# Kernel optimization log

Hardware: AMD Instinct MI355X
Metric: run time of the kernel (lower is better)

The kernel has to match this reference:

```python
import jax, jax.numpy as jnp
import numpy as np
import math

B, T, C = 1, 2048, 2048
NH, HS = 16, 128          # hs = C // nh
NLQ, NLKV, DHR = 1536, 512, 64


def _rope(x, cos, sin):
    # x: [B, T, H, D]; cos/sin: [T, D//2]. Rotates pairs (even, odd) like
    # torch's complex-multiply apply_rotary_emb.
    xr = x.reshape(x.shape[:-1] + (-1, 2))
    x_re, x_im = xr[..., 0], xr[..., 1]
    c = cos[None, :, None, :]
    s = sin[None, :, None, :]
    out = jnp.stack([x_re * c - x_im * s, x_re * s + x_im * c], axis=-1)
    return out.reshape(x.shape)


def setup_inputs() -> dict:
    key = jax.random.key(0)
    ks = jax.random.split(key, 9)
    sc = 0.02  # init scale so logits stay sane
    x = jax.random.normal(ks[0], (B, T, C), jnp.float32)
    # RoPE tables (theta = 10000), matching precompute_freqs_cis
    inv = 1.0 / (10000.0 ** (jnp.arange(0, DHR, 2, dtype=jnp.float32) / DHR))
    ang = jnp.outer(jnp.arange(T, dtype=jnp.float32), inv)  # [T, DHR//2]
    return {
        "x": x,
        "freqs_cos": jnp.cos(ang),
        "freqs_sin": jnp.sin(ang),
        "W_dq": jax.random.normal(ks[1], (NLQ, C), jnp.float32) * sc,
        "W_uq": jax.random.normal(ks[2], (C, NLQ), jnp.float32) * sc,
        "W_dkv": jax.random.normal(ks[3], (NLKV, C), jnp.float32) * sc,
        "W_uk": jax.random.normal(ks[4], (C, NLKV), jnp.float32) * sc,
        "W_uv": jax.random.normal(ks[5], (C, NLKV), jnp.float32) * sc,
        "W_qr": jax.random.normal(ks[6], (NH * DHR, NLQ), jnp.float32) * sc,
        "W_kr": jax.random.normal(ks[7], (DHR, C), jnp.float32) * sc,
        "W_o": jax.random.normal(ks[8], (C, C), jnp.float32) * sc,
    }


def reference(x, freqs_cos, freqs_sin, W_dq, W_uq, W_dkv, W_uk, W_uv, W_qr, W_kr, W_o):
    # ---- low-rank query/kv down-projections ----
    c_q = x @ W_dq.T                       # [B,T,NLQ]
    c_kv = x @ W_dkv.T                     # [B,T,NLKV]  (no kv_cache: c_kv = new_c_kv)

    # ---- weight absorption (training path) ----
    # torch: W_uq.weight.view(1,nlq,nh,hs).transpose(1,2) @ W_uk.weight.view(1,nh,hs,nlkv)
    Wuq_h = W_uq.reshape(NLQ, NH, HS).transpose(1, 0, 2)   # [NH,NLQ,HS]
    Wuk_h = W_uk.reshape(NH, HS, NLKV)                     # [NH,HS,NLKV]
    k_eff = jnp.einsum('hql,hlk->hqk', Wuq_h, Wuk_h)       # [NH,NLQ,NLKV]
    # torch: (W_uv.weight.T @ W_o.weight.T).view(nlkv,nh,hs).transpose(0,1)
    v_eff = (W_uv.T @ W_o.T).reshape(NLKV, NH, HS).transpose(1, 0, 2)  # [NH,NLKV,HS]

    # ---- content attention scores in latent space ----
    attn_c = jnp.einsum('bhtk,bsk->bhts',
                        jnp.einsum('btq,hqk->bhtk', c_q, k_eff), c_kv)  # [B,NH,T,T]

    # ---- decoupled RoPE subspace ----
    k_r = _rope((x @ W_kr.T)[:, :, None, :], freqs_cos, freqs_sin)[:, :, 0, :]   # [B,T,DHR]
    q_r = _rope((c_q @ W_qr.T).reshape(B, T, NH, DHR), freqs_cos, freqs_sin)
    q_r = q_r.transpose(0, 2, 1, 3)                                              # [B,NH,T,DHR]
    attn_r = jnp.einsum('bhtd,bsd->bhts', q_r, k_r)                              # [B,NH,T,T]

    # ---- combine, causal mask, softmax ----
    scale = 1.0 / math.sqrt(HS + DHR)
    scores = (attn_c + attn_r) * scale
    causal = jnp.tril(jnp.ones((T, T), dtype=bool))  # mask = triu(diag=1) complement
    scores = jnp.where(causal[None, None], scores, jnp.float32(-jnp.inf))
    attn = jax.nn.softmax(scores, axis=-1)           # dropout p=0.0

    # ---- value path: attend in latent space, then absorbed up+output proj ----
    y_lat = jnp.einsum('bhts,bsk->bhtk', attn, c_kv)          # [B,NH,T,NLKV]
    y = jnp.einsum('bhtk,hkd->bhtd', y_lat, v_eff)            # [B,NH,T,HS]
    y = y.transpose(0, 2, 1, 3).reshape(B, T, C)              # [B,T,C] (W_o absorbed)
    return y
```

## Files before the change

kernel.cpp:

```cpp
#include <hip/hip_runtime.h>
#include <hip/hip_bf16.h>
#include <math.h>

typedef __bf16 bf16_t;
typedef __bf16 bf16x8 __attribute__((ext_vector_type(8)));
typedef float f32x4 __attribute__((ext_vector_type(4)));

#define T_DIM 2048
#define C_DIM 2048
#define NH 16
#define HS 128
#define NLQ 1536
#define NLKV 512
#define DHR 64
#define QKD 192

__global__ void detect_k(const bf16_t* __restrict__ x, int* __restrict__ flag) {
  int bad = 0;
  for (int i = threadIdx.x; i < 256; i += 64) {
    float v = (float)x[i];
    if (!(fabsf(v) < 1.0e6f)) bad = 1;
  }
  unsigned long long m = __ballot(bad);
  if (threadIdx.x == 0) *flag = (m != 0ull) ? 1 : 0;
}

struct CvPack {
  const void* src[9];
  bf16_t* dst[9];
  int n[9];
};

__global__ __launch_bounds__(256) void convert_all_k(CvPack p, const int* __restrict__ flag) {
  const int which = blockIdx.y;
  const int n = p.n[which];
  const int f32 = *flag;
  const int stride = gridDim.x * 256 * 8;
  for (int i = (blockIdx.x * 256 + threadIdx.x) * 8; i < n; i += stride) {
    if (f32) {
      const float* s = (const float*)p.src[which] + i;
      f32x4 lo = *(const f32x4*)s;
      f32x4 hi = *(const f32x4*)(s + 4);
      bf16x8 v;
#pragma unroll
      for (int j = 0; j < 4; ++j) { v[j] = (bf16_t)lo[j]; v[j + 4] = (bf16_t)hi[j]; }
      *(bf16x8*)(p.dst[which] + i) = v;
    } else {
      *(bf16x8*)(p.dst[which] + i) = *(const bf16x8*)((const bf16_t*)p.src[which] + i);
    }
  }
}

__global__ void transpose_k(const void* __restrict__ in, bf16_t* __restrict__ out,
                            int R, int C, const int* __restrict__ flag) {
  __shared__ bf16_t tile[32][33];
  const int f32 = *flag;
  int bx = blockIdx.x * 32, by = blockIdx.y * 32;
  int tx = threadIdx.x, ty = threadIdx.y;
  for (int i = ty; i < 32; i += 8) {
    int r = by + i, c = bx + tx;
    if (r < R && c < C) {
      size_t idx = (size_t)r * C + c;
      tile[i][tx] = f32 ? (bf16_t)((const float*)in)[idx] : ((const bf16_t*)in)[idx];
    }
  }
  __syncthreads();
  for (int i = ty; i < 32; i += 8) {
    int r = bx + i, c = by + tx;
    if (r < C && c < R) out[(size_t)r * R + c] = tile[tx][i];
  }
}

__device__ __forceinline__ void async16(const bf16_t* g, bf16_t* l) {
  __builtin_amdgcn_global_load_lds(
      (const __attribute__((address_space(1))) void*)g,
      (__attribute__((address_space(3))) void*)l, 16, 0, 0);
}

#define BM 128
#define BN 128

struct GDesc {
  const bf16_t* A; const bf16_t* B; bf16_t* C;
  int M, N, K, lda, ldb, ldc, mb, bx0;
};
struct GGrp { GDesc d[3]; };

__global__ __launch_bounds__(256) void gemm_group(GGrp g, int nseg) {
  int bx = blockIdx.x;
  int s = 0;
  while (s + 1 < nseg && bx >= g.d[s + 1].bx0) ++s;
  const GDesc D = g.d[s];
  const int local = bx - D.bx0;
  const int bm = (local % D.mb) * BM, bn = (local / D.mb) * BN;

  __shared__ bf16_t As[BM * 32];
  __shared__ bf16_t Bs[BN * 32];
  const int tid = threadIdx.x;
  const int lane = tid & 63;
  const int wave = tid >> 6;
  const int l16 = lane & 15, quad = lane >> 4;
  const int wm = (wave >> 1) * 64, wn = (wave & 1) * 64;
  const int srow = lane >> 2;
  const int scol = (lane & 3) * 8;
  f32x4 acc[4][4] = {};

  for (int k0 = 0; k0 < D.K; k0 += 32) {
    __syncthreads();
#pragma unroll
    for (int pss = 0; pss < 2; ++pss) {
      int rowT = pss * 64 + wave * 16 + srow;
      int ar = bm + rowT; if (ar > D.M - 1) ar = D.M - 1;
      async16(D.A + (size_t)ar * D.lda + k0 + scol, As + (pss * 64 + wave * 16) * 32);
      int br = bn + rowT; if (br > D.N - 1) br = D.N - 1;
      async16(D.B + (size_t)br * D.ldb + k0 + scol, Bs + (pss * 64 + wave * 16) * 32);
    }
    __syncthreads();
    bf16x8 af[4], bfr[4];
#pragma unroll
    for (int i = 0; i < 4; ++i)
      af[i] = *(const bf16x8*)(As + (wm + i * 16 + l16) * 32 + quad * 8);
#pragma unroll
    for (int j = 0; j < 4; ++j)
      bfr[j] = *(const bf16x8*)(Bs + (wn + j * 16 + l16) * 32 + quad * 8);
#pragma unroll
    for (int i = 0; i < 4; ++i)
#pragma unroll
      for (int j = 0; j < 4; ++j)
        acc[i][j] = __builtin_amdgcn_mfma_f32_16x16x32_bf16(af[i], bfr[j], acc[i][j], 0, 0, 0);
  }
#pragma unroll
  for (int i = 0; i < 4; ++i)
#pragma unroll
    for (int j = 0; j < 4; ++j)
#pragma unroll
      for (int r = 0; r < 4; ++r) {
        int gm = bm + wm + i * 16 + quad * 4 + r;
        int gn = bn + wn + j * 16 + l16;
        if (gm < D.M && gn < D.N) D.C[(size_t)gm * D.ldc + gn] = (bf16_t)acc[i][j][r];
      }
}

__global__ void pack_qk_k(const bf16_t* __restrict__ qcat, const bf16_t* __restrict__ khead,
                          const bf16_t* __restrict__ xa,
                          const bf16_t* __restrict__ fc, const bf16_t* __restrict__ fs,
                          bf16_t* __restrict__ Qp, bf16_t* __restrict__ Kp) {
  int idx = blockIdx.x * blockDim.x + threadIdx.x;
  if (idx >= NH * T_DIM * 96) return;
  int j = idx % 96;
  int t = (idx / 96) % T_DIM;
  int h = idx / (96 * T_DIM);
  if (blockIdx.y == 0) {
    const float scale = 0.07216878364870323f;
    bf16_t* out = Qp + ((size_t)h * T_DIM + t) * QKD;
    if (j < 64) {
      float a = (float)qcat[(size_t)t * 3072 + h * HS + 2 * j];
      float b = (float)qcat[(size_t)t * 3072 + h * HS + 2 * j + 1];
      out[2 * j] = (bf16_t)(a * scale);
      out[2 * j + 1] = (bf16_t)(b * scale);
    } else {
      int i = j - 64;
      float re = (float)qcat[(size_t)t * 3072 + 2048 + h * DHR + 2 * i];
      float im = (float)qcat[(size_t)t * 3072 + 2048 + h * DHR + 2 * i + 1];
      float c = (float)fc[t * 32 + i], s = (float)fs[t * 32 + i];
      out[HS + 2 * i] = (bf16_t)((re * c - im * s) * scale);
      out[HS + 2 * i + 1] = (bf16_t)((re * s + im * c) * scale);
    }
  } else {
    bf16_t* out = Kp + ((size_t)h * T_DIM + t) * QKD;
    if (j < 64) {
      out[2 * j] = khead[(size_t)t * C_DIM + h * HS + 2 * j];
      out[2 * j + 1] = khead[(size_t)t * C_DIM + h * HS + 2 * j + 1];
    } else {
      int i = j - 64;
      float re = (float)xa[(size_t)t * 2112 + 2048 + 2 * i];
      float im = (float)xa[(size_t)t * 2112 + 2048 + 2 * i + 1];
      float c = (float)fc[t * 32 + i], s = (float)fs[t * 32 + i];
      out[HS + 2 * i] = (bf16_t)(re * c - im * s);
      out[HS + 2 * i + 1] = (bf16_t)(re * s + im * c);
    }
  }
}

#define FBM 128
#define FBN 64
#define KPITCH 200
#define VPITCH 72
#define PPITCH 72

__global__ __launch_bounds__(512) void flash_k(const bf16_t* __restrict__ Qp,
                                               const bf16_t* __restrict__ Kp,
                                               const bf16_t* __restrict__ VT,
                                               void* __restrict__ Y,
                                               const int* __restrict__ flag,
                                               float* __restrict__ Opart,
                                               float* __restrict__ Mpart,
                                               float* __restrict__ Lpart) {
  __shared__ bf16_t Ksm[FBN * KPITCH];
  __shared__ bf16_t Vtsm[HS * VPITCH];
  __shared__ bf16_t Psm[8][16 * PPITCH];
  const int tid = threadIdx.x;
  const int lane = tid & 63, wave = tid >> 6;
  const int l16 = lane & 15, quad = lane >> 4;
  const int h = blockIdx.y;
  const int p = blockIdx.x;
  int qt, kt0, kt1, partial;
  if (p < 16) {
    qt = 8 + (p >> 1);
    int half = qt + 1;
    kt0 = (p & 1) ? half : 0;
    kt1 = (p & 1) ? (2 * qt + 2) : half;
    partial = 1;
  } else {
    qt = 23 - p; kt0 = 0; kt1 = 2 * qt + 2; partial = 0;
  }
  const int qb = qt * FBM;
  const int f32out = *flag;

  bf16x8 aq[6];
  const bf16_t* qbase = Qp + ((size_t)h * T_DIM + qb + wave * 16 + l16) * QKD;
#pragma unroll
  for (int c = 0; c < 6; ++c) aq[c] = *(const bf16x8*)(qbase + c * 32 + quad * 8);

  f32x4 o[8] = {};
  float m_i[4], l_i[4];
#pragma unroll
  for (int r = 0; r < 4; ++r) { m_i[r] = -3.0e38f; l_i[r] = 0.f; }

  const bf16_t* kg_base = Kp + (size_t)h * T_DIM * QKD;
  const bf16_t* vg_base = VT + (size_t)(h * HS) * T_DIM;

  bf16x8 kreg[3], vreg[2];
  {
    const bf16_t* kg = kg_base + (size_t)kt0 * FBN * QKD;
#pragma unroll
    for (int i = 0; i < 3; ++i) {
      int idx = i * 512 + tid, row = idx / 24, c8 = idx % 24;
      kreg[i] = *(const bf16x8*)(kg + (size_t)row * QKD + c8 * 8);
    }
    const bf16_t* vg = vg_base + kt0 * FBN;
#pragma unroll
    for (int i = 0; i < 2; ++i) {
      int idx = i * 512 + tid, row = idx >> 3, c8 = idx & 7;
      vreg[i] = *(const bf16x8*)(vg + (size_t)row * T_DIM + c8 * 8);
    }
  }

  for (int kt = kt0; kt < kt1; ++kt) {
    __syncthreads();
#pragma unroll
    for (int i = 0; i < 3; ++i) {
      int idx = i * 512 + tid, row = idx / 24, c8 = idx % 24;
      *(bf16x8*)(Ksm + row * KPITCH + c8 * 8) = kreg[i];
    }
#pragma unroll
    for (int i = 0; i < 2; ++i) {
      int idx = i * 512 + tid, row = idx >> 3, c8 = idx & 7;
      *(bf16x8*)(Vtsm + row * VPITCH + c8 * 8) = vreg[i];
    }
    __syncthreads();
    if (kt + 1 < kt1) {
      const bf16_t* kg = kg_base + (size_t)(kt + 1) * FBN * QKD;
#pragma unroll
      for (int i = 0; i < 3; ++i) {
        int idx = i * 512 + tid, row = idx / 24, c8 = idx % 24;
        kreg[i] = *(const bf16x8*)(kg + (size_t)row * QKD + c8 * 8);
      }
      const bf16_t* vg = vg_base + (kt + 1) * FBN;
#pragma unroll
      for (int i = 0; i < 2; ++i) {
        int idx = i * 512 + tid, row = idx >> 3, c8 = idx & 7;
        vreg[i] = *(const bf16x8*)(vg + (size_t)row * T_DIM + c8 * 8);
      }
    }
    f32x4 sc[4] = {};
#pragma unroll
    for (int nt = 0; nt < 4; ++nt)
#pragma unroll
      for (int c = 0; c < 6; ++c) {
        bf16x8 bk = *(const bf16x8*)(Ksm + (nt * 16 + l16) * KPITCH + c * 32 + quad * 8);
        sc[nt] = __builtin_amdgcn_mfma_f32_16x16x32_bf16(aq[c], bk, sc[nt], 0, 0, 0);
      }
    if (kt >= 2 * qt) {
#pragma unroll
      for (int nt = 0; nt < 4; ++nt) {
        int s_glob = kt * FBN + nt * 16 + l16;
#pragma unroll
        for (int r = 0; r < 4; ++r) {
          int t_glob = qb + wave * 16 + quad * 4 + r;
          if (s_glob > t_glob) sc[nt][r] = -3.0e38f;
        }
      }
    }
    float pv_[4][4];
#pragma unroll
    for (int r = 0; r < 4; ++r) {
      float mx = fmaxf(fmaxf(sc[0][r], sc[1][r]), fmaxf(sc[2][r], sc[3][r]));
#pragma unroll
      for (int m = 1; m < 16; m <<= 1) mx = fmaxf(mx, __shfl_xor(mx, m, 64));
      float mn = fmaxf(m_i[r], mx);
      float alpha = exp2f((m_i[r] - mn) * 1.4426950408889634f);
      float rs = 0.f;
#pragma unroll
      for (int nt = 0; nt < 4; ++nt) {
        float pv = exp2f((sc[nt][r] - mn) * 1.4426950408889634f);
        pv_[nt][r] = pv;
        rs += pv;
      }
#pragma unroll
      for (int m = 1; m < 16; m <<= 1) rs += __shfl_xor(rs, m, 64);
      l_i[r] = l_i[r] * alpha + rs;
      m_i[r] = mn;
#pragma unroll
      for (int dt = 0; dt < 8; ++dt) o[dt][r] *= alpha;
    }
#pragma unroll
    for (int nt = 0; nt < 4; ++nt)
#pragma unroll
      for (int r = 0; r < 4; ++r)
        Psm[wave][(quad * 4 + r) * PPITCH + nt * 16 + l16] = (bf16_t)pv_[nt][r];
#pragma unroll
    for (int s2 = 0; s2 < 2; ++s2) {
      bf16x8 ap = *(const bf16x8*)(&Psm[wave][l16 * PPITCH + s2 * 32 + quad * 8]);
#pragma unroll
      for (int dt = 0; dt < 8; ++dt) {
        bf16x8 bv = *(const bf16x8*)(Vtsm + (dt * 16 + l16) * VPITCH + s2 * 32 + quad * 8);
        o[dt] = __builtin_amdgcn_mfma_f32_16x16x32_bf16(ap, bv, o[dt], 0, 0, 0);
      }
    }
  }

  if (!partial) {
#pragma unroll
    for (int r = 0; r < 4; ++r) {
      float inv = 1.0f / l_i[r];
      int t = qb + wave * 16 + quad * 4 + r;
#pragma unroll
      for (int dt = 0; dt < 8; ++dt) {
        size_t oi = (size_t)t * C_DIM + h * HS + dt * 16 + l16;
        float val = o[dt][r] * inv;
        if (f32out) ((float*)Y)[oi] = val;
        else        ((bf16_t*)Y)[oi] = (bf16_t)val;
      }
    }
  } else {
    const int pi = h * 16 + p;
#pragma unroll
    for (int r = 0; r < 4; ++r) {
      int rowl = wave * 16 + quad * 4 + r;
      float* ob = Opart + ((size_t)pi * 128 + rowl) * 128;
#pragma unroll
      for (int dt = 0; dt < 8; ++dt) ob[dt * 16 + l16] = o[dt][r];
      if (l16 == 0) {
        Mpart[(size_t)pi * 128 + rowl] = m_i[r];
        Lpart[(size_t)pi * 128 + rowl] = l_i[r];
      }
    }
  }
}

__global__ __launch_bounds__(256) void combine_k(const float* __restrict__ Opart,
                                                 const float* __restrict__ Mpart,
                                                 const float* __restrict__ Lpart,
                                                 void* __restrict__ Y,
                                                 const int* __restrict__ flag) {
  const int h = blockIdx.y;
  const int qi = blockIdx.x;
  const int pi0 = h * 16 + qi * 2, pi1 = pi0 + 1;
  const int row = threadIdx.x >> 1;
  const int c0 = (threadIdx.x & 1) * 64;
  const int f32out = *flag;
  float m0 = Mpart[(size_t)pi0 * 128 + row], m1 = Mpart[(size_t)pi1 * 128 + row];
  float l0 = Lpart[(size_t)pi0 * 128 + row], l1 = Lpart[(size_t)pi1 * 128 + row];
  float ms = fmaxf(m0, m1);
  float w0 = exp2f((m0 - ms) * 1.4426950408889634f);
  float w1 = exp2f((m1 - ms) * 1.4426950408889634f);
  float inv = 1.0f / (l0 * w0 + l1 * w1);
  const float* O0 = Opart + ((size_t)pi0 * 128 + row) * 128 + c0;
  const float* O1 = Opart + ((size_t)pi1 * 128 + row) * 128 + c0;
  int t = (8 + qi) * 128 + row;
  size_t ob = (size_t)t * C_DIM + h * HS + c0;
#pragma unroll
  for (int d4 = 0; d4 < 64; d4 += 4) {
    f32x4 a = *(const f32x4*)(O0 + d4);
    f32x4 b = *(const f32x4*)(O1 + d4);
#pragma unroll
    for (int j = 0; j < 4; ++j) {
      float v = (a[j] * w0 + b[j] * w1) * inv;
      if (f32out) ((float*)Y)[ob + d4 + j] = v;
      else        ((bf16_t*)Y)[ob + d4 + j] = (bf16_t)v;
    }
  }
}

extern "C" void kernel_launch(void* const* d_in, const int* in_sizes, int n_in,
                              void* d_out, int out_size, void* d_ws, size_t ws_size,
                              hipStream_t stream) {
  bf16_t* w = (bf16_t*)d_ws;
  int* flag = (int*)d_ws;

  if (ws_size < (size_t)34472000 * 2 + 128) return;

  bf16_t* fcc    = w + 64;
  bf16_t* fsc    = w + 65600;
  bf16_t* xc     = w + 131136;
  bf16_t* BigB   = w + 4325440;
  bf16_t* dqc    = BigB;
  bf16_t* dkvc   = BigB + 3145728;
  bf16_t* krc    = BigB + 4194304;
  bf16_t* Bq     = w + 8650816;
  bf16_t* W_uq_t = Bq;
  bf16_t* qrc    = Bq + 3145728;
  bf16_t* xa     = w + 13369408;
  bf16_t* qcat   = w + 17694784;
  bf16_t* k_head = w + 23986240;
  bf16_t* vhatT  = w + 28180544;
  bf16_t* ukc    = w + 32374848;
  bf16_t* Pt     = w + 33423424;
  bf16_t* woc    = qcat;
  bf16_t* W_uv_t = k_head;
  bf16_t* Qpack  = xc;
  bf16_t* Kpack  = qcat;
  float* Opart = (float*)(w + 6422592);
  float* Mpart = (float*)(w + 14811200);
  float* Lpart = (float*)(w + 14876736);

  detect_k<<<1, 64, 0, stream>>>((const bf16_t*)d_in[0], flag);

  CvPack cp;
  const void* srcs[9] = {d_in[1], d_in[2], d_in[0], d_in[3], d_in[5], d_in[9], d_in[8], d_in[6], d_in[10]};
  bf16_t* dsts[9]     = {fcc,     fsc,     xc,      dqc,     dkvc,    krc,     qrc,     ukc,     woc};
  int ns[9] = {T_DIM * 32, T_DIM * 32, T_DIM * C_DIM, NLQ * C_DIM, NLKV * C_DIM,
               DHR * C_DIM, NH * DHR * NLQ, C_DIM * NLKV, C_DIM * C_DIM};
  for (int i = 0; i < 9; ++i) { cp.src[i] = srcs[i]; cp.dst[i] = dsts[i]; cp.n[i] = ns[i]; }
  convert_all_k<<<dim3(512, 9), 256, 0, stream>>>(cp, flag);

  dim3 tb(32, 8);
  transpose_k<<<dim3(64, 48), tb, 0, stream>>>(d_in[4], W_uq_t, 1536, 2048, flag);
  transpose_k<<<dim3(16, 64), tb, 0, stream>>>(d_in[7], W_uv_t, 2048, 512, flag);

  {
    GGrp g;
    g.d[0] = {xc,  BigB,   xa, 2048, 2112, 2048, 2048, 2048, 2112, 16, 0};
    g.d[1] = {woc, W_uv_t, Pt, 2048,  512, 2048, 2048, 2048,  512, 16, 272};
    gemm_group<<<336, 256, 0, stream>>>(g, 2);
  }
  {
    GGrp g;
    g.d[0] = {xa,        Bq,        qcat,   2048, 3072, 1536, 2112, 1536, 3072, 16, 0};
    g.d[1] = {xa + 1536, ukc,       k_head, 2048, 2048,  512, 2112,  512, 2048, 16, 384};
    g.d[2] = {Pt,        xa + 1536, vhatT,  2048, 2048,  512,  512, 2112, 2048, 16, 640};
    gemm_group<<<896, 256, 0, stream>>>(g, 3);
  }

  int pk = (NH * T_DIM * 96 + 255) / 256;
  pack_qk_k<<<dim3(pk, 2), 256, 0, stream>>>(qcat, k_head, xa, fcc, fsc, Qpack, Kpack);

  flash_k<<<dim3(24, NH), 512, 0, stream>>>(Qpack, Kpack, vhatT, d_out, flag, Opart, Mpart, Lpart);
  combine_k<<<dim3(8, NH), 256, 0, stream>>>(Opart, Mpart, Lpart, d_out, flag);
}
```

Baseline: 378.2 us.

## Give each flash wave two query tiles and transpose MFMA operands

The flash attention kernel drops from 8 waves to 4, and each wave now handles 32 query rows (two 16-row MFMA tiles). Each K/V fragment read from LDS therefore feeds two MFMAs. Swapping the MFMA operand order puts query rows along lanes, so row max and row sum need only two cross-lane shuffles, and P and the outputs can be stored as packed vectors. The cost is roughly double the accumulator and Q registers per thread and fewer waves per block to hide latency.

```diff
diff --git a/kernel.cpp b/kernel.cpp
--- a/kernel.cpp
+++ b/kernel.cpp
@@ -3,6 +3,7 @@
 #include <math.h>
 
 typedef __bf16 bf16_t;
+typedef __bf16 bf16x4 __attribute__((ext_vector_type(4)));
 typedef __bf16 bf16x8 __attribute__((ext_vector_type(8)));
 typedef float f32x4 __attribute__((ext_vector_type(4)));
 
@@ -188,7 +189,7 @@
 #define VPITCH 72
 #define PPITCH 72
 
-__global__ __launch_bounds__(512) void flash_k(const bf16_t* __restrict__ Qp,
+__global__ __launch_bounds__(256) void flash_k(const bf16_t* __restrict__ Qp,
                                                const bf16_t* __restrict__ Kp,
                                                const bf16_t* __restrict__ VT,
                                                void* __restrict__ Y,
@@ -198,7 +199,7 @@
                                                float* __restrict__ Lpart) {
   __shared__ bf16_t Ksm[FBN * KPITCH];
   __shared__ bf16_t Vtsm[HS * VPITCH];
-  __shared__ bf16_t Psm[8][16 * PPITCH];
+  __shared__ bf16_t Psm[4][32 * PPITCH];
   const int tid = threadIdx.x;
   const int lane = tid & 63, wave = tid >> 6;
   const int l16 = lane & 15, quad = lane >> 4;
@@ -217,31 +218,32 @@
   const int qb = qt * FBM;
   const int f32out = *flag;
 
-  bf16x8 aq[6];
-  const bf16_t* qbase = Qp + ((size_t)h * T_DIM + qb + wave * 16 + l16) * QKD;
-#pragma unroll
-  for (int c = 0; c < 6; ++c) aq[c] = *(const bf16x8*)(qbase + c * 32 + quad * 8);
-
-  f32x4 o[8] = {};
-  float m_i[4], l_i[4];
-#pragma unroll
-  for (int r = 0; r < 4; ++r) { m_i[r] = -3.0e38f; l_i[r] = 0.f; }
+  bf16x8 aq[2][6];
+#pragma unroll
+  for (int tt = 0; tt < 2; ++tt) {
+    const bf16_t* qbase = Qp + ((size_t)h * T_DIM + qb + wave * 32 + tt * 16 + l16) * QKD;
+#pragma unroll
+    for (int c = 0; c < 6; ++c) aq[tt][c] = *(const bf16x8*)(qbase + c * 32 + quad * 8);
+  }
+
+  f32x4 o[2][8] = {};
+  float m_i[2] = {-3.0e38f, -3.0e38f}, l_i[2] = {0.f, 0.f};
 
   const bf16_t* kg_base = Kp + (size_t)h * T_DIM * QKD;
   const bf16_t* vg_base = VT + (size_t)(h * HS) * T_DIM;
 
-  bf16x8 kreg[3], vreg[2];
+  bf16x8 kreg[6], vreg[4];
   {
     const bf16_t* kg = kg_base + (size_t)kt0 * FBN * QKD;
 #pragma unroll
-    for (int i = 0; i < 3; ++i) {
-      int idx = i * 512 + tid, row = idx / 24, c8 = idx % 24;
-      kreg[i] = *(const bf16x8*)(kg + (size_t)row * QKD + c8 * 8);
+    for (int i = 0; i < 6; ++i) {
+      int idx = i * 256 + tid;
+      kreg[i] = *(const bf16x8*)(kg + (size_t)idx * 8);
     }
     const bf16_t* vg = vg_base + kt0 * FBN;
 #pragma unroll
-    for (int i = 0; i < 2; ++i) {
-      int idx = i * 512 + tid, row = idx >> 3, c8 = idx & 7;
+    for (int i = 0; i < 4; ++i) {
+      int idx = i * 256 + tid, row = idx >> 3, c8 = idx & 7;
       vreg[i] = *(const bf16x8*)(vg + (size_t)row * T_DIM + c8 * 8);
     }
   }
@@ -249,111 +251,130 @@
   for (int kt = kt0; kt < kt1; ++kt) {
     __syncthreads();
 #pragma unroll
-    for (int i = 0; i < 3; ++i) {
-      int idx = i * 512 + tid, row = idx / 24, c8 = idx % 24;
+    for (int i = 0; i < 6; ++i) {
+      int idx = i * 256 + tid, row = idx / 24, c8 = idx % 24;
       *(bf16x8*)(Ksm + row * KPITCH + c8 * 8) = kreg[i];
     }
 #pragma unroll
-    for (int i = 0; i < 2; ++i) {
-      int idx = i * 512 + tid, row = idx >> 3, c8 = idx & 7;
+    for (int i = 0; i < 4; ++i) {
+      int idx = i * 256 + tid, row = idx >> 3, c8 = idx & 7;
       *(bf16x8*)(Vtsm + row * VPITCH + c8 * 8) = vreg[i];
     }
     __syncthreads();
     if (kt + 1 < kt1) {
       const bf16_t* kg = kg_base + (size_t)(kt + 1) * FBN * QKD;
 #pragma unroll
-      for (int i = 0; i < 3; ++i) {
-        int idx = i * 512 + tid, row = idx / 24, c8 = idx % 24;
-        kreg[i] = *(const bf16x8*)(kg + (size_t)row * QKD + c8 * 8);
+      for (int i = 0; i < 6; ++i) {
+        int idx = i * 256 + tid;
+        kreg[i] = *(const bf16x8*)(kg + (size_t)idx * 8);
       }
       const bf16_t* vg = vg_base + (kt + 1) * FBN;
 #pragma unroll
-      for (int i = 0; i < 2; ++i) {
-        int idx = i * 512 + tid, row = idx >> 3, c8 = idx & 7;
+      for (int i = 0; i < 4; ++i) {
+        int idx = i * 256 + tid, row = idx >> 3, c8 = idx & 7;
         vreg[i] = *(const bf16x8*)(vg + (size_t)row * T_DIM + c8 * 8);
       }
     }
-    f32x4 sc[4] = {};
+    f32x4 sc[2][4] = {};
 #pragma unroll
     for (int nt = 0; nt < 4; ++nt)
 #pragma unroll
       for (int c = 0; c < 6; ++c) {
         bf16x8 bk = *(const bf16x8*)(Ksm + (nt * 16 + l16) * KPITCH + c * 32 + quad * 8);
-        sc[nt] = __builtin_amdgcn_mfma_f32_16x16x32_bf16(aq[c], bk, sc[nt], 0, 0, 0);
+        sc[0][nt] = __builtin_amdgcn_mfma_f32_16x16x32_bf16(bk, aq[0][c], sc[0][nt], 0, 0, 0);
+        sc[1][nt] = __builtin_amdgcn_mfma_f32_16x16x32_bf16(bk, aq[1][c], sc[1][nt], 0, 0, 0);
       }
     if (kt >= 2 * qt) {
 #pragma unroll
+      for (int tt = 0; tt < 2; ++tt) {
+        int t_glob = qb + wave * 32 + tt * 16 + l16;
+#pragma unroll
+        for (int nt = 0; nt < 4; ++nt) {
+          int s_base = kt * FBN + nt * 16 + quad * 4;
+#pragma unroll
+          for (int r = 0; r < 4; ++r)
+            if (s_base + r > t_glob) sc[tt][nt][r] = -3.0e38f;
+        }
+      }
+    }
+#pragma unroll
+    for (int tt = 0; tt < 2; ++tt) {
+      float mx = sc[tt][0][0];
+#pragma unroll
+      for (int nt = 0; nt < 4; ++nt)
+#pragma unroll
+        for (int r = 0; r < 4; ++r) mx = fmaxf(mx, sc[tt][nt][r]);
+      mx = fmaxf(mx, __shfl_xor(mx, 16, 64));
+      mx = fmaxf(mx, __shfl_xor(mx, 32, 64));
+      float mn = fmaxf(m_i[tt], mx);
+      float alpha = exp2f((m_i[tt] - mn) * 1.4426950408889634f);
+      float rs = 0.f;
+#pragma unroll
       for (int nt = 0; nt < 4; ++nt) {
-        int s_glob = kt * FBN + nt * 16 + l16;
+        bf16x4 pk;
 #pragma unroll
         for (int r = 0; r < 4; ++r) {
-          int t_glob = qb + wave * 16 + quad * 4 + r;
-          if (s_glob > t_glob) sc[nt][r] = -3.0e38f;
+          float pv = exp2f((sc[tt][nt][r] - mn) * 1.4426950408889634f);
+          rs += pv;
+          pk[r] = (bf16_t)pv;
         }
-      }
-    }
-    float pv_[4][4];
-#pragma unroll
-    for (int r = 0; r < 4; ++r) {
-      float mx = fmaxf(fmaxf(sc[0][r], sc[1][r]), fmaxf(sc[2][r], sc[3][r]));
-#pragma unroll
-      for (int m = 1; m < 16; m <<= 1) mx = fmaxf(mx, __shfl_xor(mx, m, 64));
-      float mn = fmaxf(m_i[r], mx);
-      float alpha = exp2f((m_i[r] - mn) * 1.4426950408889634f);
-      float rs = 0.f;
-#pragma unroll
-      for (int nt = 0; nt < 4; ++nt) {
-        float pv = exp2f((sc[nt][r] - mn) * 1.4426950408889634f);
-        pv_[nt][r] = pv;
-        rs += pv;
-      }
-#pragma unroll
-      for (int m = 1; m < 16; m <<= 1) rs += __shfl_xor(rs, m, 64);
-      l_i[r] = l_i[r] * alpha + rs;
-      m_i[r] = mn;
-#pragma unroll
-      for (int dt = 0; dt < 8; ++dt) o[dt][r] *= alpha;
-    }
-#pragma unroll
-    for (int nt = 0; nt < 4; ++nt)
-#pragma unroll
-      for (int r = 0; r < 4; ++r)
-        Psm[wave][(quad * 4 + r) * PPITCH + nt * 16 + l16] = (bf16_t)pv_[nt][r];
+        *(bf16x4*)(&Psm[wave][(tt * 16 + l16) * PPITCH + nt * 16 + quad * 4]) = pk;
+      }
+      rs += __shfl_xor(rs, 16, 64);
+      rs += __shfl_xor(rs, 32, 64);
+      l_i[tt] = l_i[tt] * alpha + rs;
+      m_i[tt] = mn;
+#pragma unroll
+      for (int dt = 0; dt < 8; ++dt) o[tt][dt] *= alpha;
+    }
 #pragma unroll
     for (int s2 = 0; s2 < 2; ++s2) {
-      bf16x8 ap = *(const bf16x8*)(&Psm[wave][l16 * PPITCH + s2 * 32 + quad * 8]);
+      bf16x8 ap0 = *(const bf16x8*)(&Psm[wave][l16 * PPITCH + s2 * 32 + quad * 8]);
+      bf16x8 ap1 = *(const bf16x8*)(&Psm[wave][(16 + l16) * PPITCH + s2 * 32 + quad * 8]);
 #pragma unroll
       for (int dt = 0; dt < 8; ++dt) {
         bf16x8 bv = *(const bf16x8*)(Vtsm + (dt * 16 + l16) * VPITCH + s2 * 32 + quad * 8);
-        o[dt] = __builtin_amdgcn_mfma_f32_16x16x32_bf16(ap, bv, o[dt], 0, 0, 0);
+        o[0][dt] = __builtin_amdgcn_mfma_f32_16x16x32_bf16(bv, ap0, o[0][dt], 0, 0, 0);
+        o[1][dt] = __builtin_amdgcn_mfma_f32_16x16x32_bf16(bv, ap1, o[1][dt], 0, 0, 0);
       }
     }
   }
 
   if (!partial) {
 #pragma unroll
-    for (int r = 0; r < 4; ++r) {
-      float inv = 1.0f / l_i[r];
-      int t = qb + wave * 16 + quad * 4 + r;
+    for (int tt = 0; tt < 2; ++tt) {
+      float inv = 1.0f / l_i[tt];
+      int t = qb + wave * 32 + tt * 16 + l16;
 #pragma unroll
       for (int dt = 0; dt < 8; ++dt) {
-        size_t oi = (size_t)t * C_DIM + h * HS + dt * 16 + l16;
-        float val = o[dt][r] * inv;
-        if (f32out) ((float*)Y)[oi] = val;
-        else        ((bf16_t*)Y)[oi] = (bf16_t)val;
+        size_t oi = (size_t)t * C_DIM + h * HS + dt * 16 + quad * 4;
+        if (f32out) {
+          f32x4 v;
+#pragma unroll
+          for (int r = 0; r < 4; ++r) v[r] = o[tt][dt][r] * inv;
+          *(f32x4*)((float*)Y + oi) = v;
+        } else {
+          bf16x4 v;
+#pragma unroll
+          for (int r = 0; r < 4; ++r) v[r] = (bf16_t)(o[tt][dt][r] * inv);
+          *(bf16x4*)((bf16_t*)Y + oi) = v;
+        }
       }
     }
   } else {
     const int pi = h * 16 + p;
 #pragma unroll
-    for (int r = 0; r < 4; ++r) {
-      int rowl = wave * 16 + quad * 4 + r;
+    for (int tt = 0; tt < 2; ++tt) {
+      int rowl = wave * 32 + tt * 16 + l16;
       float* ob = Opart + ((size_t)pi * 128 + rowl) * 128;
 #pragma unroll
-      for (int dt = 0; dt < 8; ++dt) ob[dt * 16 + l16] = o[dt][r];
-      if (l16 == 0) {
-        Mpart[(size_t)pi * 128 + rowl] = m_i[r];
-        Lpart[(size_t)pi * 128 + rowl] = l_i[r];
+      for (int dt = 0; dt < 8; ++dt) {
+        f32x4 v = o[tt][dt];
+        *(f32x4*)(ob + dt * 16 + quad * 4) = v;
+      }
+      if (quad == 0) {
+        Mpart[(size_t)pi * 128 + rowl] = m_i[tt];
+        Lpart[(size_t)pi * 128 + rowl] = l_i[tt];
       }
     }
   }
@@ -456,6 +477,6 @@
   int pk = (NH * T_DIM * 96 + 255) / 256;
   pack_qk_k<<<dim3(pk, 2), 256, 0, stream>>>(qcat, k_head, xa, fcc, fsc, Qpack, Kpack);
 
-  flash_k<<<dim3(24, NH), 512, 0, stream>>>(Qpack, Kpack, vhatT, d_out, flag, Opart, Mpart, Lpart);
+  flash_k<<<dim3(24, NH), 256, 0, stream>>>(Qpack, Kpack, vhatT, d_out, flag, Opart, Mpart, Lpart);
   combine_k<<<dim3(8, NH), 256, 0, stream>>>(Opart, Mpart, Lpart, d_out, flag);
 }
```

Measured after the change: 364.2 us. 1.04x faster.
